# Optimization experiments

Hardware: AMD Instinct MI355X
Metric: run time of the kernel (lower is better)

## Reference

```python
import jax, jax.numpy as jnp
import numpy as np

B, T, IN, H, NH = 64, 512, 1024, 1024, 4
HD = H // NH  # head_dim = 256
NG = 3        # gates: z (update), r (reset), n (candidate)


def setup_inputs() -> dict:
    key = jax.random.key(0)
    k1, k2, k3, k4, k5 = jax.random.split(key, 5)
    inp = jax.random.normal(k1, (B, T, IN), dtype=jnp.float32)
    # nn.Linear(input_size, 3*hidden_size): weight [3H, IN], bias [3H]
    W = jax.random.normal(k2, (IN, NG * H), dtype=jnp.float32) / np.sqrt(IN)
    bW = jax.random.normal(k3, (NG * H,), dtype=jnp.float32) * 0.02
    # recurrent R: [num_heads, head_dim_in, num_gates, head_dim_out], std=1/sqrt(head_dim)
    R = jax.random.normal(k4, (NH, HD, NG, HD), dtype=jnp.float32) / np.sqrt(HD)
    b = jax.random.normal(k5, (NH, NG, HD), dtype=jnp.float32)
    return {"input": inp, "W": W, "bW": bW, "R": R, "b": b}


def _gru_scan(Wx, R, b, h0):
    # Wx: [T, B, NH, NG, HD], h0: [B, NH, HD]
    def step(h, wx):
        # recurrent gate preactivations: Ry[b,h,g,o] = sum_i h[b,h,i] R[h,i,g,o]
        ry = jnp.einsum('bhi,higo->bhgo', h, R)
        z = jax.nn.sigmoid(wx[:, :, 0] + ry[:, :, 0] + b[:, 0])
        r = jax.nn.sigmoid(wx[:, :, 1] + ry[:, :, 1] + b[:, 1])
        n = jnp.tanh(wx[:, :, 2] + r * ry[:, :, 2] + b[:, 2])
        h_new = z * h + (1.0 - z) * n
        return h_new, h_new

    h_last, hs = jax.lax.scan(step, h0, Wx)
    return hs, h_last  # hs: [T, B, NH, HD]


def reference(input, W, bW, R, b):
    bs, sl = input.shape[0], input.shape[1]
    # input projection for all timesteps at once
    Wx = input @ W + bW                               # [B, T, NG*H]
    Wx = Wx.reshape(bs, sl, NG, NH, HD)
    Wx = jnp.transpose(Wx, (1, 0, 3, 2, 4))           # [T, B, NH, NG, HD]
    h0 = jnp.zeros((bs, NH, HD), dtype=input.dtype)
    hs, h_last = _gru_scan(Wx, R, b, h0)
    h = jnp.transpose(hs, (1, 0, 2, 3)).reshape(bs, sl, H)   # [B, T, H]
    hn = h_last.reshape(1, bs, H)                             # [num_layers=1, B, H]
    return h, hn
```

## Files before the change

kernel.cpp:

```cpp
#include <hip/hip_runtime.h>
#include <hip/hip_fp16.h>


typedef _Float16 f16x8 __attribute__((ext_vector_type(8)));
typedef _Float16 f16x2 __attribute__((ext_vector_type(2)));
typedef float    f32x4 __attribute__((ext_vector_type(4)));

#define AS1 __attribute__((address_space(1)))
#define AS3 __attribute__((address_space(3)))

__device__ __forceinline__ void async_ld16(const void* g, void* l) {
    __builtin_amdgcn_global_load_lds((const AS1 void*)g, (AS3 void*)l, 16, 0, 0);
}

__device__ __forceinline__ float sigmoidf_(float x) {
    return 1.f / (1.f + __expf(-x));
}
__device__ __forceinline__ float tanhf_(float x) {
    float e = __expf(-2.f * fabsf(x));
    float r = (1.f - e) / (1.f + e);
    return copysignf(r, x);
}

#if defined(__has_builtin)
#if __has_builtin(__builtin_amdgcn_fdot2)
#define HAVE_FDOT2 1
#endif
#endif
__device__ __forceinline__ float dot2f(f16x2 a, f16x2 b, float c) {
#ifdef HAVE_FDOT2
    return __builtin_amdgcn_fdot2(a, b, c, false);
#else
    return c + (float)a[0] * (float)b[0] + (float)a[1] * (float)b[1];
#endif
}

__global__ __launch_bounds__(256) void cast_to_f16(const float* __restrict__ in,
                                                   _Float16* __restrict__ out, int n8) {
    int i = blockIdx.x * 256 + threadIdx.x;
    if (i >= n8) return;
    const float4* p = (const float4*)in;
    float4 a = p[2 * i], b = p[2 * i + 1];
    f16x8 r;
    r[0] = (_Float16)a.x; r[1] = (_Float16)a.y; r[2] = (_Float16)a.z; r[3] = (_Float16)a.w;
    r[4] = (_Float16)b.x; r[5] = (_Float16)b.y; r[6] = (_Float16)b.z; r[7] = (_Float16)b.w;
    *(f16x8*)(out + (size_t)i * 8) = r;
}

__global__ __launch_bounds__(256) void transpose_cast(const float* __restrict__ W,
                                                      _Float16* __restrict__ WT) {
    __shared__ float tile[32][33];
    const int tx = threadIdx.x, ty = threadIdx.y;
    const int n0 = blockIdx.x * 32, k0 = blockIdx.y * 32;
#pragma unroll
    for (int j = 0; j < 32; j += 8)
        tile[ty + j][tx] = W[(size_t)(k0 + ty + j) * 3072 + n0 + tx];
    __syncthreads();
#pragma unroll
    for (int j = 0; j < 32; j += 8)
        WT[(size_t)(n0 + ty + j) * 1024 + k0 + tx] = (_Float16)tile[tx][ty + j];
}

__global__ __launch_bounds__(256) void gemm_wx(const _Float16* __restrict__ A,
                                               const _Float16* __restrict__ BT,
                                               const float* __restrict__ bW,
                                               const float* __restrict__ bR,
                                               float* __restrict__ Wx) {
    __shared__ _Float16 As[128 * 32];
    __shared__ _Float16 Bs[128 * 32];
    const int tid  = threadIdx.x;
    const int wave = tid >> 6, lane = tid & 63;
    const int m0 = blockIdx.y * 128, n0 = blockIdx.x * 128;
    const int wm = (wave >> 1) * 64, wn = (wave & 1) * 64;
    const int r16 = lane & 15, kq = lane >> 4;

    f32x4 acc[4][4];
#pragma unroll
    for (int m = 0; m < 4; m++)
#pragma unroll
        for (int n = 0; n < 4; n++) acc[m][n] = (f32x4){0.f, 0.f, 0.f, 0.f};

    const int srow = wave * 32 + (lane >> 2);
    const int scol = (lane & 3) * 8;

    for (int kt = 0; kt < 32; kt++) {
        const int k0 = kt * 32;
#pragma unroll
        for (int j = 0; j < 2; j++) {
            async_ld16(A  + (size_t)(m0 + srow + j * 16) * 1024 + k0 + scol,
                       As + (wave * 32 + j * 16) * 32);
            async_ld16(BT + (size_t)(n0 + srow + j * 16) * 1024 + k0 + scol,
                       Bs + (wave * 32 + j * 16) * 32);
        }
        __syncthreads();
        f16x8 af[4], bf[4];
#pragma unroll
        for (int m = 0; m < 4; m++) af[m] = *(const f16x8*)(As + (wm + m * 16 + r16) * 32 + kq * 8);
#pragma unroll
        for (int n = 0; n < 4; n++) bf[n] = *(const f16x8*)(Bs + (wn + n * 16 + r16) * 32 + kq * 8);
#pragma unroll
        for (int m = 0; m < 4; m++)
#pragma unroll
            for (int n = 0; n < 4; n++)
                acc[m][n] = __builtin_amdgcn_mfma_f32_16x16x32_f16(af[m], bf[n], acc[m][n], 0, 0, 0);
        __syncthreads();
    }

#pragma unroll
    for (int m = 0; m < 4; m++) {
        const int row0 = m0 + wm + m * 16 + (lane >> 4) * 4;
#pragma unroll
        for (int n = 0; n < 4; n++) {
            const int col  = n0 + wn + n * 16 + r16;
            const int g    = col >> 10, head = (col >> 8) & 3, o = col & 255;
            const float bias = bW[col] + bR[head * 768 + g * 256 + o];
#pragma unroll
            for (int q = 0; q < 4; q++) {
                const int rr = row0 + q;
                const int t = rr & 511, bb = rr >> 9;
                Wx[(((size_t)t * 64 + bb) * 12 + head * 3 + g) * 256 + o] = acc[m][n][q] + bias;
            }
        }
    }
}

__global__ __attribute__((amdgpu_waves_per_eu(2, 2)))
__launch_bounds__(512) void scan_persist(const float* __restrict__ R,
                                         const float* __restrict__ Wx,
                                         float* __restrict__ out) {
    const int head = blockIdx.x >> 6;
    const int b    = blockIdx.x & 63;
    const int t    = threadIdx.x;
    const int o    = t & 255;
    const int ih   = t >> 8;

    __shared__ _Float16 h16[256];
    __shared__ float red[2][3][256];

    f16x2 Rr[3][64];
    {
        const float* Rb = R + (((size_t)head * 256 + ih * 128) * 3) * 256 + o;
#pragma unroll
        for (int i2 = 0; i2 < 64; i2++) {
#pragma unroll
            for (int g = 0; g < 3; g++) {
                const float lo = Rb[((size_t)(2 * i2) * 3 + g) * 256];
                const float hi = Rb[((size_t)(2 * i2 + 1) * 3 + g) * 256];
                f16x2 p; p[0] = (_Float16)lo; p[1] = (_Float16)hi;
                Rr[g][i2] = p;
            }
        }
    }

    float hreg = 0.f;
    float wxc0 = 0.f, wxc1 = 0.f, wxc2 = 0.f;
    if (t < 256) {
        const float* p = Wx + ((size_t)b * 12 + head * 3) * 256 + o;
        wxc0 = p[0]; wxc1 = p[256]; wxc2 = p[512];
        h16[o] = (_Float16)0.f;
    }
    __syncthreads();

    float* outp = out + (size_t)b * 512 * 1024 + head * 256 + o;

    for (int step = 0; step < 512; step++) {
        float wxn0 = 0.f, wxn1 = 0.f, wxn2 = 0.f;
        if (t < 256 && step < 511) {
            const float* p = Wx + (((size_t)(step + 1) * 64 + b) * 12 + head * 3) * 256 + o;
            wxn0 = p[0]; wxn1 = p[256]; wxn2 = p[512];
        }
        float az = 0.f, ar = 0.f, an = 0.f;
        const f16x8* hp = (const f16x8*)(h16 + ih * 128);
#pragma unroll
        for (int k = 0; k < 16; k++) {
            union { f16x8 v; f16x2 p[4]; } u;
            u.v = hp[k];
#pragma unroll
            for (int j = 0; j < 4; j++) {
                az = dot2f(Rr[0][k * 4 + j], u.p[j], az);
                ar = dot2f(Rr[1][k * 4 + j], u.p[j], ar);
                an = dot2f(Rr[2][k * 4 + j], u.p[j], an);
            }
        }
        red[ih][0][o] = az; red[ih][1][o] = ar; red[ih][2][o] = an;
        __syncthreads();
        if (t < 256) {
            const float z  = sigmoidf_(wxc0 + red[0][0][o] + red[1][0][o]);
            const float r  = sigmoidf_(wxc1 + red[0][1][o] + red[1][1][o]);
            const float n  = tanhf_(wxc2 + r * (red[0][2][o] + red[1][2][o]));
            const float hn = z * hreg + (1.f - z) * n;
            hreg = hn;
            outp[(size_t)step * 1024] = hn;
            h16[o] = (_Float16)hn;
        }
        wxc0 = wxn0; wxc1 = wxn1; wxc2 = wxn2;
        __syncthreads();
    }
}

__global__ __launch_bounds__(256) void copy_hn(float* __restrict__ out) {
    const int idx = blockIdx.x * 256 + threadIdx.x;
    out[(size_t)64 * 512 * 1024 + idx] =
        out[((size_t)(idx >> 10) * 512 + 511) * 1024 + (idx & 1023)];
}

extern "C" void kernel_launch(void* const* d_in, const int* in_sizes, int n_in,
                              void* d_out, int out_size, void* d_ws, size_t ws_size,
                              hipStream_t stream) {
    (void)in_sizes; (void)n_in; (void)out_size; (void)ws_size;
    const float* inp = (const float*)d_in[0];
    const float* W   = (const float*)d_in[1];
    const float* bW  = (const float*)d_in[2];
    const float* R   = (const float*)d_in[3];
    const float* bR  = (const float*)d_in[4];
    float* out = (float*)d_out;

    _Float16* A16 = (_Float16*)d_ws;
    _Float16* WT  = (_Float16*)((char*)d_ws + 67108864);
    float*    Wx  = (float*)((char*)d_ws + 73400320);

    cast_to_f16<<<16384, 256, 0, stream>>>(inp, A16, 4194304);
    transpose_cast<<<dim3(96, 32), dim3(32, 8), 0, stream>>>(W, WT);
    gemm_wx<<<dim3(24, 256), 256, 0, stream>>>(A16, WT, bW, bR, Wx);
    scan_persist<<<256, 512, 0, stream>>>(R, Wx, out);
    copy_hn<<<256, 256, 0, stream>>>(out);
}
```

Measured before the change: 1.074 ms.

## Split scan reduction across 1024 threads and stage candidate-gate weights in LDS

The recurrent scan block grows from 512 to 1024 threads, so each thread reduces over 64 inputs instead of 128. The z and r gate weights stay in registers, while the candidate-gate weights are moved into dynamic LDS in a padded transposed layout. The goal is to shorten the serial dot-product chain per timestep and cut register pressure. In exchange, the final combine now sums four partials instead of two, and each step adds LDS reads for the n-gate weights plus more threads taking part in each barrier.

```diff
diff --git a/kernel.cpp b/kernel.cpp
--- a/kernel.cpp
+++ b/kernel.cpp
@@ -124,31 +124,36 @@
     }
 }
 
-__global__ __attribute__((amdgpu_waves_per_eu(2, 2)))
-__launch_bounds__(512) void scan_persist(const float* __restrict__ R,
-                                         const float* __restrict__ Wx,
-                                         float* __restrict__ out) {
+__global__ __launch_bounds__(1024) void scan_persist(const float* __restrict__ R,
+                                                     const float* __restrict__ Wx,
+                                                     float* __restrict__ out) {
+    extern __shared__ char smem[];
+    _Float16* h16 = (_Float16*)smem;
+    float*    red = (float*)(smem + 512);
+    _Float16* Rn  = (_Float16*)(smem + 512 + 12288);
+
     const int head = blockIdx.x >> 6;
     const int b    = blockIdx.x & 63;
     const int t    = threadIdx.x;
     const int o    = t & 255;
     const int ih   = t >> 8;
 
-    __shared__ _Float16 h16[256];
-    __shared__ float red[2][3][256];
-
-    f16x2 Rr[3][64];
+    for (int idx = t; idx < 65536; idx += 1024) {
+        const int i = idx >> 8, o2 = idx & 255;
+        Rn[o2 * 264 + i] = (_Float16)R[(((size_t)head * 256 + i) * 3 + 2) * 256 + o2];
+    }
+
+    f16x2 Rz[32], Rq[32];
     {
-        const float* Rb = R + (((size_t)head * 256 + ih * 128) * 3) * 256 + o;
-#pragma unroll
-        for (int i2 = 0; i2 < 64; i2++) {
-#pragma unroll
-            for (int g = 0; g < 3; g++) {
-                const float lo = Rb[((size_t)(2 * i2) * 3 + g) * 256];
-                const float hi = Rb[((size_t)(2 * i2 + 1) * 3 + g) * 256];
-                f16x2 p; p[0] = (_Float16)lo; p[1] = (_Float16)hi;
-                Rr[g][i2] = p;
-            }
+        const float* Rb = R + (((size_t)head * 256 + ih * 64) * 3) * 256 + o;
+#pragma unroll
+        for (int i2 = 0; i2 < 32; i2++) {
+            f16x2 pz, pq;
+            pz[0] = (_Float16)Rb[((size_t)(2 * i2) * 3 + 0) * 256];
+            pz[1] = (_Float16)Rb[((size_t)(2 * i2 + 1) * 3 + 0) * 256];
+            pq[0] = (_Float16)Rb[((size_t)(2 * i2) * 3 + 1) * 256];
+            pq[1] = (_Float16)Rb[((size_t)(2 * i2 + 1) * 3 + 1) * 256];
+            Rz[i2] = pz; Rq[i2] = pq;
         }
     }
 
@@ -162,6 +167,7 @@
     __syncthreads();
 
     float* outp = out + (size_t)b * 512 * 1024 + head * 256 + o;
+    const _Float16* RnRow = Rn + o * 264 + ih * 64;
 
     for (int step = 0; step < 512; step++) {
         float wxn0 = 0.f, wxn1 = 0.f, wxn2 = 0.f;
@@ -170,24 +176,31 @@
             wxn0 = p[0]; wxn1 = p[256]; wxn2 = p[512];
         }
         float az = 0.f, ar = 0.f, an = 0.f;
-        const f16x8* hp = (const f16x8*)(h16 + ih * 128);
-#pragma unroll
-        for (int k = 0; k < 16; k++) {
-            union { f16x8 v; f16x2 p[4]; } u;
+        const f16x8* hp = (const f16x8*)(h16 + ih * 64);
+        const f16x8* np = (const f16x8*)RnRow;
+#pragma unroll
+        for (int k = 0; k < 8; k++) {
+            union { f16x8 v; f16x2 p[4]; } u, w;
             u.v = hp[k];
+            w.v = np[k];
 #pragma unroll
             for (int j = 0; j < 4; j++) {
-                az = dot2f(Rr[0][k * 4 + j], u.p[j], az);
-                ar = dot2f(Rr[1][k * 4 + j], u.p[j], ar);
-                an = dot2f(Rr[2][k * 4 + j], u.p[j], an);
+                az = dot2f(Rz[k * 4 + j], u.p[j], az);
+                ar = dot2f(Rq[k * 4 + j], u.p[j], ar);
+                an = dot2f(w.p[j],        u.p[j], an);
             }
         }
-        red[ih][0][o] = az; red[ih][1][o] = ar; red[ih][2][o] = an;
+        red[(ih * 3 + 0) * 256 + o] = az;
+        red[(ih * 3 + 1) * 256 + o] = ar;
+        red[(ih * 3 + 2) * 256 + o] = an;
         __syncthreads();
         if (t < 256) {
-            const float z  = sigmoidf_(wxc0 + red[0][0][o] + red[1][0][o]);
-            const float r  = sigmoidf_(wxc1 + red[0][1][o] + red[1][1][o]);
-            const float n  = tanhf_(wxc2 + r * (red[0][2][o] + red[1][2][o]));
+            const float sz = red[o] + red[768 + o] + red[1536 + o] + red[2304 + o];
+            const float sr = red[256 + o] + red[1024 + o] + red[1792 + o] + red[2560 + o];
+            const float sn = red[512 + o] + red[1280 + o] + red[2048 + o] + red[2816 + o];
+            const float z  = sigmoidf_(wxc0 + sz);
+            const float r  = sigmoidf_(wxc1 + sr);
+            const float n  = tanhf_(wxc2 + r * sn);
             const float hn = z * hreg + (1.f - z) * n;
             hreg = hn;
             outp[(size_t)step * 1024] = hn;
@@ -219,9 +232,13 @@
     _Float16* WT  = (_Float16*)((char*)d_ws + 67108864);
     float*    Wx  = (float*)((char*)d_ws + 73400320);
 
+    const int scan_lds = 512 + 12288 + 256 * 264 * 2;
+    hipFuncSetAttribute((const void*)scan_persist,
+                        hipFuncAttributeMaxDynamicSharedMemorySize, scan_lds);
+
     cast_to_f16<<<16384, 256, 0, stream>>>(inp, A16, 4194304);
     transpose_cast<<<dim3(96, 32), dim3(32, 8), 0, stream>>>(W, WT);
     gemm_wx<<<dim3(24, 256), 256, 0, stream>>>(A16, WT, bW, bR, Wx);
-    scan_persist<<<256, 512, 0, stream>>>(R, Wx, out);
+    scan_persist<<<256, 1024, scan_lds, stream>>>(R, Wx, out);
     copy_hn<<<256, 256, 0, stream>>>(out);
 }
```

New measurement: 1.034 ms. -3.8%, faster.
